# Kernel optimization log

Hardware: AMD Instinct MI355X
Metric: run time of the kernel (lower is better)

The kernel has to match this reference:

```python
import jax, jax.numpy as jnp
import numpy as np

K = 3          # kernel size (implied by 18/27 offset channels)
PAD = 1
STRIDE = 1


def setup_inputs() -> dict:
    key = jax.random.key(0)
    k0, k1, k2 = jax.random.split(key, 3)
    B, C, H, W = 4, 256, 64, 64
    Cout = 256
    x = jax.random.normal(k0, (B, C, H, W), jnp.float32)
    # offset/mask predicting conv: 18 offset + 9 mask channels (deform_group=1)
    w_off = jax.random.normal(k1, (27, C, K, K), jnp.float32) * 0.01
    b_off = jnp.zeros((27,), jnp.float32)
    # main deformable conv weight (bias=False)
    w = jax.random.normal(k2, (Cout, C, K, K), jnp.float32) * 0.05
    return {"x": x, "w_off": w_off, "b_off": b_off, "w": w}


def _modulated_dcn(x, w_off, b_off, w):
    B, C, H, W = x.shape
    KK = K * K
    # regular conv predicting offsets (+ mask)
    om = jax.lax.conv_general_dilated(
        x, w_off, (STRIDE, STRIDE), [(PAD, PAD), (PAD, PAD)],
        dimension_numbers=("NCHW", "OIHW", "NCHW")) + b_off[None, :, None, None]
    Ho, Wo = om.shape[2], om.shape[3]
    # channel layout: interleaved (dy, dx) per kernel tap, then 9 mask channels
    off = om[:, :2 * KK].reshape(B, KK, 2, Ho, Wo)
    mask = jax.nn.sigmoid(om[:, 2 * KK:3 * KK])            # (B, KK, Ho, Wo)

    ky, kx = jnp.meshgrid(jnp.arange(K), jnp.arange(K), indexing="ij")
    base_y = (jnp.arange(Ho) * STRIDE - PAD)[:, None]       # (Ho, 1)
    base_x = (jnp.arange(Wo) * STRIDE - PAD)[None, :]       # (1, Wo)
    # sampling positions p = p0 + pn + offset, shape (B, KK, Ho, Wo)
    py = base_y[None, None] + ky.reshape(KK)[None, :, None, None] + off[:, :, 0]
    px = base_x[None, None] + kx.reshape(KK)[None, :, None, None] + off[:, :, 1]

    y0f = jnp.floor(py)
    x0f = jnp.floor(px)
    ly = py - y0f
    lx = px - x0f
    y0 = y0f.astype(jnp.int32)
    x0 = x0f.astype(jnp.int32)

    xf = x.reshape(B, C, H * W)

    def samp(yi, xi):
        valid = ((yi >= 0) & (yi < H) & (xi >= 0) & (xi < W)).astype(x.dtype)
        idx = jnp.clip(yi, 0, H - 1) * W + jnp.clip(xi, 0, W - 1)
        v = jnp.take_along_axis(xf, idx.reshape(B, 1, -1), axis=2)
        return v.reshape(B, C, KK, Ho, Wo) * valid[:, None]

    # bilinear interpolation with zero padding outside the image
    v = (samp(y0,     x0    ) * ((1 - ly) * (1 - lx))[:, None]
         + samp(y0,     x0 + 1) * ((1 - ly) * lx)[:, None]
         + samp(y0 + 1, x0    ) * (ly * (1 - lx))[:, None]
         + samp(y0 + 1, x0 + 1) * (ly * lx)[:, None])
    v = v * mask[:, None]                                   # modulation
    # conv as contraction over (Cin, KK)
    return jnp.einsum("bckhw,ock->bohw", v, w.reshape(w.shape[0], C, KK))


def reference(x, w_off, b_off, w):
    return _modulated_dcn(x, w_off, b_off, w)
```

## Files before the change

kernel.cpp:

```cpp
#include <hip/hip_runtime.h>
#include <math.h>

#define HH 64
#define WW 64
#define CIN 256
#define COUT 256
#define KKT 9
#define HWSZ 4096
#define VP 260
#define TP 264

typedef __bf16  v8bf   __attribute__((ext_vector_type(8)));
typedef float   v4f    __attribute__((ext_vector_type(4)));
typedef short   short8 __attribute__((ext_vector_type(8)));
typedef unsigned short ushort4v __attribute__((ext_vector_type(4)));
typedef unsigned short ushort8v __attribute__((ext_vector_type(8)));

__device__ inline unsigned short f2bf(float f) {
    union { float f; unsigned u; } uf; uf.f = f;
    unsigned r = uf.u + 0x7fff + ((uf.u >> 16) & 1);
    return (unsigned short)(r >> 16);
}
__device__ inline float bf2f(unsigned short u) {
    union { unsigned u; float f; } uf; uf.u = ((unsigned)u) << 16;
    return uf.f;
}

__global__ __launch_bounds__(256) void k_prep(const float* __restrict__ x,
                                              const float* __restrict__ w,
                                              const float* __restrict__ w_off,
                                              unsigned short* __restrict__ x_t,
                                              unsigned short* __restrict__ wprep,
                                              unsigned short* __restrict__ woffp) {
    __shared__ __align__(16) unsigned short s_t[32 * TP];
    int id  = blockIdx.x;
    int tid = threadIdx.x;
    if (id < 512) {
        int b    = id >> 7;
        int r    = id & 127;
        int h    = r >> 1;
        int half = r & 1;
        const float* xr = x + ((size_t)b * CIN) * HWSZ + h * WW + half * 32;
#pragma unroll
        for (int it = 0; it < 8; it++) {
            int idx = it * 256 + tid;
            int c   = idx >> 3;
            int p4  = idx & 7;
            float4 v = *(const float4*)(xr + (size_t)c * HWSZ + p4 * 4);
            s_t[(p4 * 4 + 0) * TP + c] = f2bf(v.x);
            s_t[(p4 * 4 + 1) * TP + c] = f2bf(v.y);
            s_t[(p4 * 4 + 2) * TP + c] = f2bf(v.z);
            s_t[(p4 * 4 + 3) * TP + c] = f2bf(v.w);
        }
        __syncthreads();
        unsigned short* orow = x_t + (((size_t)(b * 64 + h)) * WW + half * 32) * CIN;
#pragma unroll
        for (int it = 0; it < 4; it++) {
            int idx = it * 256 + tid;
            int px  = idx >> 5;
            int c8  = (idx & 31) * 8;
            *(short8*)(orow + (size_t)px * CIN + c8) = *(const short8*)&s_t[px * TP + c8];
        }
    } else if (id < 768) {
        float* s_w = (float*)s_t;
        int o = id - 512;
        for (int i = tid; i < 2304; i += 256) s_w[i] = w[(size_t)o * 2304 + i];
        __syncthreads();
        for (int u = tid; u < 576; u += 256) {
            int t  = u >> 3;
            int kq = u & 7;
            unsigned short v[4];
#pragma unroll
            for (int j = 0; j < 4; j++) {
                int kp = t * 32 + kq * 4 + j;
                int kk = kp >> 8;
                int c  = kp & 255;
                v[j] = f2bf(s_w[c * 9 + kk]);
            }
            *(ushort4v*)&wprep[((size_t)(t * 256 + o)) * 32 + kq * 4] = *(ushort4v*)v;
        }
    } else {
        int t = id - 768;
#pragma unroll
        for (int i = 0; i < 4; i++) {
            int idx = i * 256 + tid;
            int och = idx >> 5;
            int ki  = idx & 31;
            int kp  = t * 32 + ki;
            int kk  = kp >> 8;
            int c   = kp & 255;
            float v = (och < 27) ? w_off[((size_t)och * 256 + c) * 9 + kk] : 0.f;
            woffp[(size_t)t * 1024 + idx] = f2bf(v);
        }
    }
}

__global__ __launch_bounds__(256) void k_off_mfma(const unsigned short* __restrict__ x_t,
                                                  const unsigned short* __restrict__ woffp,
                                                  const float* __restrict__ b_off,
                                                  float* __restrict__ om) {
    int id    = blockIdx.x;
    int g     = id & 7;
    int phalf = (id >> 3) & 1;
    int hi    = (id >> 4) & 7;
    int b     = id >> 7;
    int h     = g * 8 + hi;
    int p0    = phalf * 32;
    int tid  = threadIdx.x;
    int lane = tid & 63;
    int wv   = tid >> 6;
    int g2   = wv >> 1;
    int ntw  = wv & 1;
    int m16  = lane & 15;
    int quad = lane >> 4;

    __shared__ unsigned short s_row[3 * 34 * VP];
    __shared__ float s_red[2][32][33];

    const unsigned short* xb = x_t + (size_t)b * HWSZ * CIN;

    for (int u = tid; u < 3 * 1088; u += 256) {
        int row = u / 1088;
        int rem = u - row * 1088;
        int px  = rem >> 5;
        int c8  = (rem & 31) * 8;
        int y   = h + row - 1;
        int xg  = p0 + px - 1;
        short8 val = (short8)0;
        if ((unsigned)y < HH && (unsigned)xg < WW)
            val = *(const short8*)(xb + ((size_t)y * WW + xg) * CIN + c8);
        *(short8*)&s_row[(row * 34 + px) * VP + c8] = val;
    }
    __syncthreads();

    v4f acc[2];
    acc[0] = (v4f)(0.f);
    acc[1] = (v4f)(0.f);

#pragma unroll
    for (int ky = 0; ky < 3; ky++) {
#pragma unroll
        for (int kx = 0; kx < 3; kx++) {
#pragma unroll
            for (int c2 = 0; c2 < 4; c2++) {
                int ch = c2 * 2 + g2;
                int t  = (ky * 3 + kx) * 8 + ch;
                const unsigned short* wp = woffp + (size_t)t * 1024;
                short8 af0 = *(const short8*)(wp + m16 * 32 + quad * 8);
                short8 af1 = *(const short8*)(wp + (16 + m16) * 32 + quad * 8);
                short8 bfr = *(const short8*)
                    &s_row[(ky * 34 + ntw * 16 + m16 + kx) * VP + ch * 32 + quad * 8];
                acc[0] = __builtin_amdgcn_mfma_f32_16x16x32_bf16(
                    __builtin_bit_cast(v8bf, af0), __builtin_bit_cast(v8bf, bfr), acc[0], 0, 0, 0);
                acc[1] = __builtin_amdgcn_mfma_f32_16x16x32_bf16(
                    __builtin_bit_cast(v8bf, af1), __builtin_bit_cast(v8bf, bfr), acc[1], 0, 0, 0);
            }
        }
    }

#pragma unroll
    for (int mt = 0; mt < 2; mt++)
#pragma unroll
        for (int r = 0; r < 4; r++)
            s_red[g2][mt * 16 + quad * 4 + r][ntw * 16 + m16] = acc[mt][r];
    __syncthreads();

    for (int i2 = tid; i2 < 27 * 32; i2 += 256) {
        int och = i2 >> 5;
        int px  = i2 & 31;
        float s = s_red[0][och][px] + s_red[1][och][px] + b_off[och];
        om[((size_t)b * 27 + och) * HWSZ + h * WW + p0 + px] = s;
    }
}

__global__ __launch_bounds__(512, 4) void k_main(const unsigned short* __restrict__ x_t,
                                                 const float* __restrict__ om,
                                                 const unsigned short* __restrict__ wprep,
                                                 float* __restrict__ out) {
    int id    = blockIdx.x;
    int g     = id & 7;
    int phalf = (id >> 3) & 1;
    int hi    = (id >> 4) & 7;
    int b     = id >> 7;
    int h     = g * 8 + hi;
    int p0    = phalf * 32;
    int tid  = threadIdx.x;
    int lane = tid & 63;
    int oct  = tid >> 6;
    int m16  = lane & 15;
    int quad = lane >> 4;
    int hsel = lane >> 5;
    int l32  = lane & 31;

    __shared__ int4   s_base[KKT][32];
    __shared__ float4 s_wt  [KKT][32];
    __shared__ __align__(16) unsigned short s_v[32 * VP];

    const float* omb = om + (size_t)b * 27 * HWSZ + h * WW;
    for (int i = tid; i < KKT * 32; i += 512) {
        int kk = i >> 5;
        int pl = i & 31;
        int p  = p0 + pl;
        float offy = omb[(size_t)(2 * kk)     * HWSZ + p];
        float offx = omb[(size_t)(2 * kk + 1) * HWSZ + p];
        float mv   = omb[(size_t)(18 + kk)    * HWSZ + p];
        int ky = kk / 3, kx = kk - 3 * (kk / 3);
        float py = (float)(h - 1 + ky) + offy;
        float px = (float)(p - 1 + kx) + offx;
        float y0f = floorf(py);
        float x0f = floorf(px);
        float ly = py - y0f, lx = px - x0f;
        int y0 = (int)y0f, x0 = (int)x0f;
        float m = 1.f / (1.f + __expf(-mv));
        bool yv0 = (unsigned)y0       < HH;
        bool yv1 = (unsigned)(y0 + 1) < HH;
        bool xv0 = (unsigned)x0       < WW;
        bool xv1 = (unsigned)(x0 + 1) < WW;
        int y0c = min(max(y0, 0), HH - 1);
        int y1c = min(max(y0 + 1, 0), HH - 1);
        int x0c = min(max(x0, 0), WW - 1);
        int x1c = min(max(x0 + 1, 0), WW - 1);
        s_base[kk][pl] = make_int4((y0c * WW + x0c) * CIN, (y0c * WW + x1c) * CIN,
                                   (y1c * WW + x0c) * CIN, (y1c * WW + x1c) * CIN);
        s_wt[kk][pl] = make_float4(
            (yv0 && xv0) ? (1.f - ly) * (1.f - lx) * m : 0.f,
            (yv0 && xv1) ? (1.f - ly) * lx         * m : 0.f,
            (yv1 && xv0) ? ly * (1.f - lx)         * m : 0.f,
            (yv1 && xv1) ? ly * lx                 * m : 0.f);
    }
    __syncthreads();

    v4f acc[2][2];
#pragma unroll
    for (int mt = 0; mt < 2; mt++)
#pragma unroll
        for (int nt = 0; nt < 2; nt++) acc[mt][nt] = (v4f)(0.f);

    const unsigned short* xb = x_t + (size_t)b * HWSZ * CIN;
    const unsigned short* xcf = xb + l32 * 8;

    for (int kk = 0; kk < KKT; kk++) {
        int pl0 = oct * 4 + hsel;
        int pl1 = oct * 4 + 2 + hsel;
        int4   bp0 = s_base[kk][pl0];
        int4   bp1 = s_base[kk][pl1];
        ushort8v ta0 = *(const ushort8v*)(xcf + bp0.x);
        ushort8v ta1 = *(const ushort8v*)(xcf + bp0.y);
        ushort8v ta2 = *(const ushort8v*)(xcf + bp0.z);
        ushort8v ta3 = *(const ushort8v*)(xcf + bp0.w);
        ushort8v tb0 = *(const ushort8v*)(xcf + bp1.x);
        ushort8v tb1 = *(const ushort8v*)(xcf + bp1.y);
        ushort8v tb2 = *(const ushort8v*)(xcf + bp1.z);
        ushort8v tb3 = *(const ushort8v*)(xcf + bp1.w);
        float4 wt0 = s_wt[kk][pl0];
        float4 wt1 = s_wt[kk][pl1];
        {
            unsigned short vv[8];
#pragma unroll
            for (int j = 0; j < 8; j++) {
                float val = wt0.x * bf2f(ta0[j]) + wt0.y * bf2f(ta1[j])
                          + wt0.z * bf2f(ta2[j]) + wt0.w * bf2f(ta3[j]);
                vv[j] = f2bf(val);
            }
            *(ushort8v*)&s_v[pl0 * VP + l32 * 8] = *(ushort8v*)vv;
        }
        {
            unsigned short vv[8];
#pragma unroll
            for (int j = 0; j < 8; j++) {
                float val = wt1.x * bf2f(tb0[j]) + wt1.y * bf2f(tb1[j])
                          + wt1.z * bf2f(tb2[j]) + wt1.w * bf2f(tb3[j]);
                vv[j] = f2bf(val);
            }
            *(ushort8v*)&s_v[pl1 * VP + l32 * 8] = *(ushort8v*)vv;
        }
        __syncthreads();

#pragma unroll 2
        for (int ch = 0; ch < 8; ch++) {
            int t = kk * 8 + ch;
            const unsigned short* wp = wprep + ((size_t)t * 256 + oct * 32) * 32;
            short8 af0 = *(const short8*)(wp + m16 * 32 + quad * 8);
            short8 af1 = *(const short8*)(wp + (16 + m16) * 32 + quad * 8);
            short8 bfr[2];
#pragma unroll
            for (int nt = 0; nt < 2; nt++)
                bfr[nt] = *(const short8*)&s_v[(nt * 16 + m16) * VP + ch * 32 + quad * 8];
#pragma unroll
            for (int nt = 0; nt < 2; nt++) {
                acc[0][nt] = __builtin_amdgcn_mfma_f32_16x16x32_bf16(
                    __builtin_bit_cast(v8bf, af0), __builtin_bit_cast(v8bf, bfr[nt]),
                    acc[0][nt], 0, 0, 0);
                acc[1][nt] = __builtin_amdgcn_mfma_f32_16x16x32_bf16(
                    __builtin_bit_cast(v8bf, af1), __builtin_bit_cast(v8bf, bfr[nt]),
                    acc[1][nt], 0, 0, 0);
            }
        }
        __syncthreads();
    }

    float* ob = out + ((size_t)b * COUT) * HWSZ + h * WW + p0;
#pragma unroll
    for (int mt = 0; mt < 2; mt++)
#pragma unroll
        for (int nt = 0; nt < 2; nt++)
#pragma unroll
            for (int r = 0; r < 4; r++) {
                int o = oct * 32 + mt * 16 + quad * 4 + r;
                ob[(size_t)o * HWSZ + nt * 16 + m16] = acc[mt][nt][r];
            }
}

extern "C" void kernel_launch(void* const* d_in, const int* in_sizes, int n_in,
                              void* d_out, int out_size, void* d_ws, size_t ws_size,
                              hipStream_t stream) {
    const float* x     = (const float*)d_in[0];
    const float* w_off = (const float*)d_in[1];
    const float* b_off = (const float*)d_in[2];
    const float* w     = (const float*)d_in[3];
    float* out = (float*)d_out;

    float* om = (float*)d_ws;
    unsigned short* x_t   = (unsigned short*)(om + 442368);
    unsigned short* wprep = x_t + (size_t)4 * HWSZ * CIN;
    unsigned short* woffp = wprep + 589824;

    hipLaunchKernelGGL(k_prep,     dim3(840), dim3(256), 0, stream, x, w, w_off, x_t, wprep, woffp);
    hipLaunchKernelGGL(k_off_mfma, dim3(512), dim3(256), 0, stream, x_t, woffp, b_off, om);
    hipLaunchKernelGGL(k_main,     dim3(512), dim3(512), 0, stream, x_t, om, wprep, out);
}
```

Measured before the change: 139.7 us.

## Double-buffer sampled tile to overlap next-tap gathers with MFMA

The shared-memory sampled-value buffer is now double-buffered. The bilinear gather loads for the next kernel tap are issued before the MFMA loop over the current tap, and the interpolated values are written to the alternate buffer afterwards. This drops one barrier per tap and hides global gather latency behind matrix work. In exchange it doubles the LDS for s_v and keeps more vector registers live across the MFMA loop, which could lower occupancy.

```diff
diff --git a/kernel.cpp b/kernel.cpp
--- a/kernel.cpp
+++ b/kernel.cpp
@@ -194,7 +194,7 @@
 
     __shared__ int4   s_base[KKT][32];
     __shared__ float4 s_wt  [KKT][32];
-    __shared__ __align__(16) unsigned short s_v[32 * VP];
+    __shared__ __align__(16) unsigned short s_v[2][32 * VP];
 
     const float* omb = om + (size_t)b * 27 * HWSZ + h * WW;
     for (int i = tid; i < KKT * 32; i += 512) {
@@ -236,14 +236,17 @@
 #pragma unroll
         for (int nt = 0; nt < 2; nt++) acc[mt][nt] = (v4f)(0.f);
 
-    const unsigned short* xb = x_t + (size_t)b * HWSZ * CIN;
+    const unsigned short* xb  = x_t + (size_t)b * HWSZ * CIN;
     const unsigned short* xcf = xb + l32 * 8;
 
-    for (int kk = 0; kk < KKT; kk++) {
-        int pl0 = oct * 4 + hsel;
-        int pl1 = oct * 4 + 2 + hsel;
-        int4   bp0 = s_base[kk][pl0];
-        int4   bp1 = s_base[kk][pl1];
+    int pl0 = oct * 4 + hsel;
+    int pl1 = oct * 4 + 2 + hsel;
+
+    {
+        int4   bp0 = s_base[0][pl0];
+        int4   bp1 = s_base[0][pl1];
+        float4 wt0 = s_wt[0][pl0];
+        float4 wt1 = s_wt[0][pl1];
         ushort8v ta0 = *(const ushort8v*)(xcf + bp0.x);
         ushort8v ta1 = *(const ushort8v*)(xcf + bp0.y);
         ushort8v ta2 = *(const ushort8v*)(xcf + bp0.z);
@@ -252,29 +255,41 @@
         ushort8v tb1 = *(const ushort8v*)(xcf + bp1.y);
         ushort8v tb2 = *(const ushort8v*)(xcf + bp1.z);
         ushort8v tb3 = *(const ushort8v*)(xcf + bp1.w);
-        float4 wt0 = s_wt[kk][pl0];
-        float4 wt1 = s_wt[kk][pl1];
-        {
-            unsigned short vv[8];
-#pragma unroll
-            for (int j = 0; j < 8; j++) {
-                float val = wt0.x * bf2f(ta0[j]) + wt0.y * bf2f(ta1[j])
-                          + wt0.z * bf2f(ta2[j]) + wt0.w * bf2f(ta3[j]);
-                vv[j] = f2bf(val);
-            }
-            *(ushort8v*)&s_v[pl0 * VP + l32 * 8] = *(ushort8v*)vv;
-        }
-        {
-            unsigned short vv[8];
-#pragma unroll
-            for (int j = 0; j < 8; j++) {
-                float val = wt1.x * bf2f(tb0[j]) + wt1.y * bf2f(tb1[j])
-                          + wt1.z * bf2f(tb2[j]) + wt1.w * bf2f(tb3[j]);
-                vv[j] = f2bf(val);
-            }
-            *(ushort8v*)&s_v[pl1 * VP + l32 * 8] = *(ushort8v*)vv;
-        }
-        __syncthreads();
+        unsigned short v0[8], v1[8];
+#pragma unroll
+        for (int j = 0; j < 8; j++) {
+            v0[j] = f2bf(wt0.x * bf2f(ta0[j]) + wt0.y * bf2f(ta1[j])
+                       + wt0.z * bf2f(ta2[j]) + wt0.w * bf2f(ta3[j]));
+            v1[j] = f2bf(wt1.x * bf2f(tb0[j]) + wt1.y * bf2f(tb1[j])
+                       + wt1.z * bf2f(tb2[j]) + wt1.w * bf2f(tb3[j]));
+        }
+        *(ushort8v*)&s_v[0][pl0 * VP + l32 * 8] = *(ushort8v*)v0;
+        *(ushort8v*)&s_v[0][pl1 * VP + l32 * 8] = *(ushort8v*)v1;
+    }
+    __syncthreads();
+
+    for (int kk = 0; kk < KKT; kk++) {
+        const unsigned short* sv = &s_v[kk & 1][0];
+        unsigned short* svn      = &s_v[(kk & 1) ^ 1][0];
+        bool more = (kk < KKT - 1);
+
+        ushort8v ta0, ta1, ta2, ta3, tb0, tb1, tb2, tb3;
+        float4 wt0, wt1;
+        if (more) {
+            int4 bp0 = s_base[kk + 1][pl0];
+            int4 bp1 = s_base[kk + 1][pl1];
+            wt0 = s_wt[kk + 1][pl0];
+            wt1 = s_wt[kk + 1][pl1];
+            ta0 = *(const ushort8v*)(xcf + bp0.x);
+            ta1 = *(const ushort8v*)(xcf + bp0.y);
+            ta2 = *(const ushort8v*)(xcf + bp0.z);
+            ta3 = *(const ushort8v*)(xcf + bp0.w);
+            tb0 = *(const ushort8v*)(xcf + bp1.x);
+            tb1 = *(const ushort8v*)(xcf + bp1.y);
+            tb2 = *(const ushort8v*)(xcf + bp1.z);
+            tb3 = *(const ushort8v*)(xcf + bp1.w);
+        }
+        __builtin_amdgcn_sched_barrier(0);
 
 #pragma unroll 2
         for (int ch = 0; ch < 8; ch++) {
@@ -285,7 +300,7 @@
             short8 bfr[2];
 #pragma unroll
             for (int nt = 0; nt < 2; nt++)
-                bfr[nt] = *(const short8*)&s_v[(nt * 16 + m16) * VP + ch * 32 + quad * 8];
+                bfr[nt] = *(const short8*)&sv[(nt * 16 + m16) * VP + ch * 32 + quad * 8];
 #pragma unroll
             for (int nt = 0; nt < 2; nt++) {
                 acc[0][nt] = __builtin_amdgcn_mfma_f32_16x16x32_bf16(
@@ -296,7 +311,21 @@
                     acc[1][nt], 0, 0, 0);
             }
         }
-        __syncthreads();
+        __builtin_amdgcn_sched_barrier(0);
+
+        if (more) {
+            unsigned short v0[8], v1[8];
+#pragma unroll
+            for (int j = 0; j < 8; j++) {
+                v0[j] = f2bf(wt0.x * bf2f(ta0[j]) + wt0.y * bf2f(ta1[j])
+                           + wt0.z * bf2f(ta2[j]) + wt0.w * bf2f(ta3[j]));
+                v1[j] = f2bf(wt1.x * bf2f(tb0[j]) + wt1.y * bf2f(tb1[j])
+                           + wt1.z * bf2f(tb2[j]) + wt1.w * bf2f(tb3[j]));
+            }
+            *(ushort8v*)&svn[pl0 * VP + l32 * 8] = *(ushort8v*)v0;
+            *(ushort8v*)&svn[pl1 * VP + l32 * 8] = *(ushort8v*)v1;
+            __syncthreads();
+        }
     }
 
     float* ob = out + ((size_t)b * COUT) * HWSZ + h * WW + p0;
```

Result: slower. 166.6 us (+19.2%).

## Widen offset conv to 512 threads and batch two taps per sync in main kernel

Applied to the files above, without the earlier changes.

The offset-conv kernel now runs 512 threads per block and splits the channel chunks across four wave groups, with a four-way shared reduction, to raise parallelism. The main kernel double-sizes its staging buffer and gathers and interpolates two kernel taps before each barrier pair. This halves the number of synchronizations and lengthens the MFMA runs between them. The cost is more LDS per block in both kernels, which may lower occupancy.

```diff
diff --git a/kernel.cpp b/kernel.cpp
--- a/kernel.cpp
+++ b/kernel.cpp
@@ -95,10 +95,10 @@
     }
 }
 
-__global__ __launch_bounds__(256) void k_off_mfma(const unsigned short* __restrict__ x_t,
-                                                  const unsigned short* __restrict__ woffp,
-                                                  const float* __restrict__ b_off,
-                                                  float* __restrict__ om) {
+__global__ __launch_bounds__(512, 4) void k_off_mfma(const unsigned short* __restrict__ x_t,
+                                                     const unsigned short* __restrict__ woffp,
+                                                     const float* __restrict__ b_off,
+                                                     float* __restrict__ om) {
     int id    = blockIdx.x;
     int g     = id & 7;
     int phalf = (id >> 3) & 1;
@@ -115,11 +115,11 @@
     int quad = lane >> 4;
 
     __shared__ unsigned short s_row[3 * 34 * VP];
-    __shared__ float s_red[2][32][33];
+    __shared__ float s_red[4][32][33];
 
     const unsigned short* xb = x_t + (size_t)b * HWSZ * CIN;
 
-    for (int u = tid; u < 3 * 1088; u += 256) {
+    for (int u = tid; u < 3 * 1088; u += 512) {
         int row = u / 1088;
         int rem = u - row * 1088;
         int px  = rem >> 5;
@@ -142,8 +142,8 @@
 #pragma unroll
         for (int kx = 0; kx < 3; kx++) {
 #pragma unroll
-            for (int c2 = 0; c2 < 4; c2++) {
-                int ch = c2 * 2 + g2;
+            for (int c2 = 0; c2 < 2; c2++) {
+                int ch = c2 * 4 + g2;
                 int t  = (ky * 3 + kx) * 8 + ch;
                 const unsigned short* wp = woffp + (size_t)t * 1024;
                 short8 af0 = *(const short8*)(wp + m16 * 32 + quad * 8);
@@ -165,10 +165,11 @@
             s_red[g2][mt * 16 + quad * 4 + r][ntw * 16 + m16] = acc[mt][r];
     __syncthreads();
 
-    for (int i2 = tid; i2 < 27 * 32; i2 += 256) {
+    for (int i2 = tid; i2 < 27 * 32; i2 += 512) {
         int och = i2 >> 5;
         int px  = i2 & 31;
-        float s = s_red[0][och][px] + s_red[1][och][px] + b_off[och];
+        float s = s_red[0][och][px] + s_red[1][och][px]
+                + s_red[2][och][px] + s_red[3][och][px] + b_off[och];
         om[((size_t)b * 27 + och) * HWSZ + h * WW + p0 + px] = s;
     }
 }
@@ -194,7 +195,7 @@
 
     __shared__ int4   s_base[KKT][32];
     __shared__ float4 s_wt  [KKT][32];
-    __shared__ __align__(16) unsigned short s_v[32 * VP];
+    __shared__ __align__(16) unsigned short s_v[2][32 * VP];
 
     const float* omb = om + (size_t)b * 27 * HWSZ + h * WW;
     for (int i = tid; i < KKT * 32; i += 512) {
@@ -236,14 +237,15 @@
 #pragma unroll
         for (int nt = 0; nt < 2; nt++) acc[mt][nt] = (v4f)(0.f);
 
-    const unsigned short* xb = x_t + (size_t)b * HWSZ * CIN;
+    const unsigned short* xb  = x_t + (size_t)b * HWSZ * CIN;
     const unsigned short* xcf = xb + l32 * 8;
 
-    for (int kk = 0; kk < KKT; kk++) {
-        int pl0 = oct * 4 + hsel;
-        int pl1 = oct * 4 + 2 + hsel;
-        int4   bp0 = s_base[kk][pl0];
-        int4   bp1 = s_base[kk][pl1];
+    int pl0 = oct * 4 + hsel;
+    int pl1 = oct * 4 + 2 + hsel;
+
+    auto stage = [&](int kki, int buf) {
+        int4   bp0 = s_base[kki][pl0];
+        int4   bp1 = s_base[kki][pl1];
         ushort8v ta0 = *(const ushort8v*)(xcf + bp0.x);
         ushort8v ta1 = *(const ushort8v*)(xcf + bp0.y);
         ushort8v ta2 = *(const ushort8v*)(xcf + bp0.z);
@@ -252,52 +254,54 @@
         ushort8v tb1 = *(const ushort8v*)(xcf + bp1.y);
         ushort8v tb2 = *(const ushort8v*)(xcf + bp1.z);
         ushort8v tb3 = *(const ushort8v*)(xcf + bp1.w);
-        float4 wt0 = s_wt[kk][pl0];
-        float4 wt1 = s_wt[kk][pl1];
-        {
-            unsigned short vv[8];
-#pragma unroll
-            for (int j = 0; j < 8; j++) {
-                float val = wt0.x * bf2f(ta0[j]) + wt0.y * bf2f(ta1[j])
-                          + wt0.z * bf2f(ta2[j]) + wt0.w * bf2f(ta3[j]);
-                vv[j] = f2bf(val);
-            }
-            *(ushort8v*)&s_v[pl0 * VP + l32 * 8] = *(ushort8v*)vv;
-        }
-        {
-            unsigned short vv[8];
-#pragma unroll
-            for (int j = 0; j < 8; j++) {
-                float val = wt1.x * bf2f(tb0[j]) + wt1.y * bf2f(tb1[j])
-                          + wt1.z * bf2f(tb2[j]) + wt1.w * bf2f(tb3[j]);
-                vv[j] = f2bf(val);
-            }
-            *(ushort8v*)&s_v[pl1 * VP + l32 * 8] = *(ushort8v*)vv;
-        }
+        float4 wt0 = s_wt[kki][pl0];
+        float4 wt1 = s_wt[kki][pl1];
+        unsigned short v0[8], v1[8];
+#pragma unroll
+        for (int j = 0; j < 8; j++) {
+            v0[j] = f2bf(wt0.x * bf2f(ta0[j]) + wt0.y * bf2f(ta1[j])
+                       + wt0.z * bf2f(ta2[j]) + wt0.w * bf2f(ta3[j]));
+            v1[j] = f2bf(wt1.x * bf2f(tb0[j]) + wt1.y * bf2f(tb1[j])
+                       + wt1.z * bf2f(tb2[j]) + wt1.w * bf2f(tb3[j]));
+        }
+        *(ushort8v*)&s_v[buf][pl0 * VP + l32 * 8] = *(ushort8v*)v0;
+        *(ushort8v*)&s_v[buf][pl1 * VP + l32 * 8] = *(ushort8v*)v1;
+    };
+
+    auto mfma_ch = [&](int t, const unsigned short* sv, int ch) {
+        const unsigned short* wp = wprep + ((size_t)t * 256 + oct * 32) * 32;
+        short8 af0 = *(const short8*)(wp + m16 * 32 + quad * 8);
+        short8 af1 = *(const short8*)(wp + (16 + m16) * 32 + quad * 8);
+        short8 bfr[2];
+#pragma unroll
+        for (int nt = 0; nt < 2; nt++)
+            bfr[nt] = *(const short8*)&sv[(nt * 16 + m16) * VP + ch * 32 + quad * 8];
+#pragma unroll
+        for (int nt = 0; nt < 2; nt++) {
+            acc[0][nt] = __builtin_amdgcn_mfma_f32_16x16x32_bf16(
+                __builtin_bit_cast(v8bf, af0), __builtin_bit_cast(v8bf, bfr[nt]),
+                acc[0][nt], 0, 0, 0);
+            acc[1][nt] = __builtin_amdgcn_mfma_f32_16x16x32_bf16(
+                __builtin_bit_cast(v8bf, af1), __builtin_bit_cast(v8bf, bfr[nt]),
+                acc[1][nt], 0, 0, 0);
+        }
+    };
+
+    for (int kp = 0; kp < 4; kp++) {
+        int kk0 = 2 * kp;
+        stage(kk0, 0);
+        stage(kk0 + 1, 1);
         __syncthreads();
-
-#pragma unroll 2
-        for (int ch = 0; ch < 8; ch++) {
-            int t = kk * 8 + ch;
-            const unsigned short* wp = wprep + ((size_t)t * 256 + oct * 32) * 32;
-            short8 af0 = *(const short8*)(wp + m16 * 32 + quad * 8);
-            short8 af1 = *(const short8*)(wp + (16 + m16) * 32 + quad * 8);
-            short8 bfr[2];
-#pragma unroll
-            for (int nt = 0; nt < 2; nt++)
-                bfr[nt] = *(const short8*)&s_v[(nt * 16 + m16) * VP + ch * 32 + quad * 8];
-#pragma unroll
-            for (int nt = 0; nt < 2; nt++) {
-                acc[0][nt] = __builtin_amdgcn_mfma_f32_16x16x32_bf16(
-                    __builtin_bit_cast(v8bf, af0), __builtin_bit_cast(v8bf, bfr[nt]),
-                    acc[0][nt], 0, 0, 0);
-                acc[1][nt] = __builtin_amdgcn_mfma_f32_16x16x32_bf16(
-                    __builtin_bit_cast(v8bf, af1), __builtin_bit_cast(v8bf, bfr[nt]),
-                    acc[1][nt], 0, 0, 0);
-            }
-        }
+#pragma unroll 4
+        for (int ci = 0; ci < 16; ci++)
+            mfma_ch(kk0 * 8 + ci, &s_v[ci >> 3][0], ci & 7);
         __syncthreads();
     }
+    stage(8, 0);
+    __syncthreads();
+#pragma unroll 4
+    for (int ch = 0; ch < 8; ch++)
+        mfma_ch(64 + ch, &s_v[0][0], ch);
 
     float* ob = out + ((size_t)b * COUT) * HWSZ + h * WW + p0;
 #pragma unroll
@@ -326,6 +330,6 @@
     unsigned short* woffp = wprep + 589824;
 
     hipLaunchKernelGGL(k_prep,     dim3(840), dim3(256), 0, stream, x, w, w_off, x_t, wprep, woffp);
-    hipLaunchKernelGGL(k_off_mfma, dim3(512), dim3(256), 0, stream, x_t, woffp, b_off, om);
+    hipLaunchKernelGGL(k_off_mfma, dim3(512), dim3(512), 0, stream, x_t, woffp, b_off, om);
     hipLaunchKernelGGL(k_main,     dim3(512), dim3(512), 0, stream, x_t, om, wprep, out);
 }
```

Measured after the change: 166.1 us. 1.19x slower.
